# Kernel optimization log

Hardware: AMD Instinct MI355X
Metric: run time of the kernel (lower is better)

## Reference

```python
import jax, jax.numpy as jnp
import numpy as np

E = 8          # num_experts
TOP_K = 2
CAP_RATIO = 1.2


def setup_inputs() -> dict:
    key = jax.random.key(0)
    k1, k2, k3, k4 = jax.random.split(key, 4)
    B, L, D, H = 2, 2048, 768, 2048
    x = jax.random.normal(k1, (B, L, D), dtype=jnp.float32)
    Wg = jax.random.normal(k2, (D, E), dtype=jnp.float32) * 0.02   # gate: Linear(D, E, bias=False)
    W1 = jax.random.normal(k3, (E, D, 2 * H), dtype=jnp.float32) * 0.02  # fc1 per expert (y | gate halves)
    W2 = jax.random.normal(k4, (E, H, D), dtype=jnp.float32) * 0.02      # fc2 per expert
    return {"x": x, "Wg": Wg, "W1": W1, "W2": W2}


def reference(x, Wg, W1, W2):
    B, L, D = x.shape
    H = W2.shape[1]
    xf = x.reshape(-1, D)                      # [N, D]
    N = xf.shape[0]
    capacity = int(CAP_RATIO * N / E)          # static, matches torch int()

    logits = xf @ Wg                           # [N, E]
    scores, idx = jax.lax.top_k(logits, TOP_K) # [N, K] (descending, like torch.topk)
    weights = jax.nn.softmax(scores, axis=-1)  # [N, K]

    # padded token table: row N is a zero token used for unfilled capacity slots
    xpad = jnp.concatenate([xf, jnp.zeros((1, D), xf.dtype)], axis=0)
    wpad_zero = jnp.zeros((1,), weights.dtype)
    out = jnp.zeros((N, D), x.dtype)

    for k in range(TOP_K):
        ik = idx[:, k]                                         # [N] expert id per token
        onehot = (ik[:, None] == jnp.arange(E)[None, :])       # [N, E]
        pos = jnp.cumsum(onehot, axis=0) - 1                   # rank within expert, ascending token order
        posk = jnp.take_along_axis(pos, ik[:, None], axis=1)[:, 0]  # [N]
        keep = posk < capacity                                 # first-come capacity (== indices[:capacity])

        # dispatch buffer [E, C]: token index per slot, N (pad) where unfilled/dropped
        buf = jnp.full((E, capacity), N, dtype=jnp.int32)
        buf = buf.at[ik, posk].set(jnp.arange(N, dtype=jnp.int32), mode="drop")

        xg = xpad[buf]                                         # [E, C, D]
        h = jnp.einsum("ecd,edh->ech", xg, W1)                 # [E, C, 2H]
        act = h[..., :H] * jax.nn.silu(h[..., H:])             # GatedMLP: y * silu(gate)
        ye = jnp.einsum("ech,ehd->ecd", act, W2)               # [E, C, D]

        wk = jnp.where(keep, weights[:, k], 0.0)               # [N]
        w_buf = jnp.concatenate([wk, wpad_zero])[buf]          # [E, C], 0 on pad slots
        out = out.at[buf.reshape(-1)].add(
            (w_buf[..., None] * ye).reshape(E * capacity, D), mode="drop"
        )

    return out.reshape(B, L, D)
```

## Files before the change

kernel.cpp:

```cpp
#include <hip/hip_runtime.h>


typedef _Float16 half8 __attribute__((ext_vector_type(8)));
typedef _Float16 half4t __attribute__((ext_vector_type(4)));
typedef float f4 __attribute__((ext_vector_type(4)));

#define N_TOK 4096
#define DDIM  768
#define HDIM  2048
#define NEXP  8
#define CAP   614
#define CAPP  640

#define XH_OFF    0L
#define W1T_OFF   6292992L
#define W2T_OFF   56624640L
#define ACT_OFF   81790464L
#define EIDX_OFF  123733504L
#define WTS_OFF   123766272L
#define TOKL_OFF  123799040L
#define CNT_OFF   123840000L

__device__ __forceinline__ void gld16(const void* g, void* l) {
  __builtin_amdgcn_global_load_lds(
      (const __attribute__((address_space(1))) unsigned int*)g,
      (__attribute__((address_space(3))) unsigned int*)l, 16, 0, 0);
}

__device__ __forceinline__ void cvt2_tile(const float* __restrict__ src,
                                          _Float16* __restrict__ dst,
                                          int R, int C, int e, int r0, int c0,
                                          float* __restrict__ tile) {
  long sb = (long)e * R * C;
  int t = threadIdx.x;
  int rrow = t >> 4, c4 = (t & 15) * 4;
#pragma unroll
  for (int h = 0; h < 2; h++)
#pragma unroll
    for (int i = 0; i < 4; i++) {
      int row = i * 16 + rrow;
      f4 v = *(const f4*)(src + sb + (long)(r0 + row) * C + c0 + h * 64 + c4);
      *(f4*)(&tile[h * 4416 + row * 69 + c4]) = v;
    }
  __syncthreads();
#pragma unroll
  for (int h = 0; h < 2; h++)
#pragma unroll
    for (int s = 0; s < 2; s++) {
      int idx = t + s * 256;
      int c = idx >> 3, ch = idx & 7;
      half8 hv;
#pragma unroll
      for (int j = 0; j < 8; j++) hv[j] = (_Float16)tile[h * 4416 + (ch * 8 + j) * 69 + c];
      *(half8*)(dst + sb + (long)(c0 + h * 64 + c) * R + r0 + ch * 8) = hv;
    }
}

__global__ __launch_bounds__(256) void prep1_kernel(const float* __restrict__ W1,
                                                    const float* __restrict__ x,
                                                    const float* __restrict__ Wg,
                                                    _Float16* __restrict__ w1t,
                                                    _Float16* __restrict__ xh,
                                                    int* __restrict__ eidx,
                                                    float* __restrict__ wts) {
  __shared__ float smem[2 * 4416];
  int b = blockIdx.x;

  if (b < 3072) {
    int e = b / 384, rem = b % 384;
    int cx = rem % 12, cy = rem / 12;
    cvt2_tile(W1, w1t, 768, 4096, e, cx * 64, cy * 128, smem);
    return;
  }

  int rb = b - 3072;
  int t = threadIdx.x;
  for (int i = t; i < DDIM * NEXP; i += 256) smem[(i & 7) * DDIM + (i >> 3)] = Wg[i];
  __syncthreads();
  int w = t >> 6, lane = t & 63;
  int tok = rb * 4 + w;
  if (tok > N_TOK) return;
  if (tok == N_TOK) {
    half4t zz; zz[0] = zz[1] = zz[2] = zz[3] = (_Float16)0.f;
#pragma unroll
    for (int j = 0; j < 3; j++) *(half4t*)(xh + (long)N_TOK * DDIM + (lane + j * 64) * 4) = zz;
    return;
  }
  const float* xr = x + (long)tok * DDIM;
#pragma unroll
  for (int j = 0; j < 3; j++) {
    f4 v = *(const f4*)(xr + (lane + j * 64) * 4);
    half4t hv;
    hv[0] = (_Float16)v[0]; hv[1] = (_Float16)v[1];
    hv[2] = (_Float16)v[2]; hv[3] = (_Float16)v[3];
    *(half4t*)(xh + (long)tok * DDIM + (lane + j * 64) * 4) = hv;
  }
  float acc[8] = {0.f, 0.f, 0.f, 0.f, 0.f, 0.f, 0.f, 0.f};
#pragma unroll
  for (int i = 0; i < 12; i++) {
    float xv = xr[i * 64 + lane];
#pragma unroll
    for (int e2 = 0; e2 < 8; e2++) acc[e2] += xv * smem[e2 * DDIM + i * 64 + lane];
  }
#pragma unroll
  for (int e2 = 0; e2 < 8; e2++) {
    float v = acc[e2];
    v += __shfl_xor(v, 32); v += __shfl_xor(v, 16); v += __shfl_xor(v, 8);
    v += __shfl_xor(v, 4);  v += __shfl_xor(v, 2);  v += __shfl_xor(v, 1);
    acc[e2] = v;
  }
  if (lane == 0) {
    float m0 = -1e30f; int i0 = 0;
#pragma unroll
    for (int e2 = 0; e2 < 8; e2++) if (acc[e2] > m0) { m0 = acc[e2]; i0 = e2; }
    float m1 = -1e30f; int i1 = 0;
#pragma unroll
    for (int e2 = 0; e2 < 8; e2++) if (e2 != i0 && acc[e2] > m1) { m1 = acc[e2]; i1 = e2; }
    float tt = __expf(m1 - m0);
    float w0 = 1.f / (1.f + tt);
    eidx[tok * 2 + 0] = i0; eidx[tok * 2 + 1] = i1;
    wts[tok * 2 + 0] = w0;  wts[tok * 2 + 1] = 1.f - w0;
  }
}

__global__ __launch_bounds__(64) void scan_kernel(const int* __restrict__ eidx,
                                                  int* __restrict__ toklist,
                                                  int* __restrict__ counts) {
  int z = blockIdx.x;
  int k = z >> 3, e = z & 7;
  int lane = threadIdx.x;
  int mye[64];
#pragma unroll
  for (int c = 0; c < 64; c++) mye[c] = eidx[(c * 64 + lane) * 2 + k];
  int base = 0;
#pragma unroll 4
  for (int c = 0; c < 64; c++) {
    int n = c * 64 + lane;
    bool pred = (mye[c] == e);
    unsigned long long mask = __ballot(pred);
    if (pred) {
      int pos = base + __popcll(mask & ((1ull << lane) - 1ull));
      if (pos < CAP) toklist[z * CAPP + pos] = n;
    }
    base += __popcll(mask);
  }
  if (lane == 0) counts[z] = (base < CAP) ? base : CAP;
}

__global__ __launch_bounds__(256, 2) void gemm1_kernel(const _Float16* __restrict__ xh,
                                                       const _Float16* __restrict__ w1t,
                                                       const float* __restrict__ W2,
                                                       _Float16* __restrict__ w2t,
                                                       const int* __restrict__ toklist,
                                                       const int* __restrict__ counts,
                                                       _Float16* __restrict__ act) {
  __shared__ char smem[49664];

  int i = blockIdx.x;
  if (i >= 1280) {
    int b2 = i - 1280;
    int e = b2 / 192, rem = b2 % 192;
    int cx = rem % 32, cy = rem / 32;
    cvt2_tile(W2, w2t, 2048, 768, e, cx * 64, cy * 128, (float*)smem);
    return;
  }

  _Float16* As = (_Float16*)smem;
  _Float16* Bs = (_Float16*)(smem + 16384);
  int* toks = (int*)(smem + 49152);

  int xcd = i & 7, j = i >> 3;
  int m = j % 5, ii = j / 5;
  int k = ii & 1, n = ii >> 1;
  int e = xcd, z = k * 8 + e;
  int count = counts[z];
  int m0 = m * 128;
  if (m0 >= count) return;
  int n0 = n * 128;

  int t = threadIdx.x;
  if (t < 128) {
    int r = m0 + t;
    toks[t] = (r < count) ? toklist[z * CAPP + r] : N_TOK;
  }
  __syncthreads();

  int lane = t & 63, w = t >> 6;
  int l8 = lane >> 3, u8 = lane & 7;

  const _Float16* ag[4]; _Float16* al[4];
#pragma unroll
  for (int s = 0; s < 4; s++) {
    int row = w * 32 + s * 8 + l8;
    ag[s] = xh + (long)toks[row] * DDIM + ((u8 ^ (row & 7)) * 8);
    al[s] = As + row * 64 + u8 * 8;
  }
  const _Float16* bg[8]; _Float16* bl[8];
#pragma unroll
  for (int s = 0; s < 8; s++) {
    int rb = w * 64 + s * 8 + l8;
    int gr = (rb < 128) ? (n0 + rb) : (2048 + n0 + (rb - 128));
    bg[s] = w1t + ((long)e * 4096 + gr) * DDIM + ((u8 ^ (rb & 7)) * 8);
    bl[s] = Bs + rb * 64 + u8 * 8;
  }

  int q = lane >> 4, m16 = lane & 15;
  int wm = w & 1, wn = w >> 1;

  f4 zero4 = {0.f, 0.f, 0.f, 0.f};
  f4 acc[4][4][2];
#pragma unroll
  for (int rt = 0; rt < 4; rt++)
#pragma unroll
    for (int ct = 0; ct < 4; ct++) { acc[rt][ct][0] = zero4; acc[rt][ct][1] = zero4; }

  for (int kk = 0; kk < DDIM; kk += 64) {
    __syncthreads();
#pragma unroll
    for (int s = 0; s < 4; s++) { gld16(ag[s], al[s]); ag[s] += 64; }
#pragma unroll
    for (int s = 0; s < 8; s++) { gld16(bg[s], bl[s]); bg[s] += 64; }
    __syncthreads();

#pragma unroll
    for (int c = 0; c < 2; c++) {
      half8 af[4], bf[4][2];
#pragma unroll
      for (int rt = 0; rt < 4; rt++) {
        int row = wm * 64 + rt * 16 + m16;
        af[rt] = *(const half8*)(As + row * 64 + (((c * 4 + q) ^ (row & 7)) * 8));
      }
#pragma unroll
      for (int ct = 0; ct < 4; ct++) {
        int cb = wn * 64 + ct * 16 + m16;
        int ph = ((c * 4 + q) ^ (cb & 7)) * 8;
        bf[ct][0] = *(const half8*)(Bs + cb * 64 + ph);
        bf[ct][1] = *(const half8*)(Bs + (128 + cb) * 64 + ph);
      }
#pragma unroll
      for (int rt = 0; rt < 4; rt++)
#pragma unroll
        for (int ct = 0; ct < 4; ct++) {
          acc[rt][ct][0] = __builtin_amdgcn_mfma_f32_16x16x32_f16(af[rt], bf[ct][0], acc[rt][ct][0], 0, 0, 0);
          acc[rt][ct][1] = __builtin_amdgcn_mfma_f32_16x16x32_f16(af[rt], bf[ct][1], acc[rt][ct][1], 0, 0, 0);
        }
    }
  }

  long ab = (long)z * CAPP * HDIM;
#pragma unroll
  for (int rt = 0; rt < 4; rt++)
#pragma unroll
    for (int ct = 0; ct < 4; ct++)
#pragma unroll
      for (int r = 0; r < 4; r++) {
        int row = m0 + wm * 64 + rt * 16 + q * 4 + r;
        int col = n0 + wn * 64 + ct * 16 + m16;
        float h1 = acc[rt][ct][0][r], h2 = acc[rt][ct][1][r];
        float s = h2 / (1.f + __expf(-h2));
        act[ab + (long)row * HDIM + col] = (_Float16)(h1 * s);
      }
}

__global__ __launch_bounds__(256, 3) void gemm2_kernel(const _Float16* __restrict__ act,
                                                       const _Float16* __restrict__ w2t,
                                                       const int* __restrict__ toklist,
                                                       const int* __restrict__ counts,
                                                       const float* __restrict__ wts,
                                                       float* __restrict__ out) {
  int i = blockIdx.x;
  int xcd = i & 7, j = i >> 3;
  int m = j % 5, t2 = j / 5;
  int k = t2 & 1, n = t2 >> 1;
  int e = xcd, z = k * 8 + e;
  int count = counts[z];
  int m0 = m * 128;
  if (m0 >= count) return;
  int n0 = n * 128;

  __shared__ _Float16 As[128 * 64];
  __shared__ _Float16 Bs[128 * 64];
  __shared__ int toksL[128];
  __shared__ float wrow[128];

  int t = threadIdx.x;
  if (t < 128) {
    int r = m0 + t;
    if (r < count) {
      int tok = toklist[z * CAPP + r];
      toksL[t] = tok;
      wrow[t] = wts[tok * 2 + k];
    } else {
      toksL[t] = -1;
      wrow[t] = 0.f;
    }
  }
  __syncthreads();

  int lane = t & 63, w = t >> 6;
  int l8 = lane >> 3, u8 = lane & 7;

  const _Float16* ag[4]; _Float16* al[4];
#pragma unroll
  for (int s = 0; s < 4; s++) {
    int row = w * 32 + s * 8 + l8;
    ag[s] = act + ((long)z * CAPP + m0 + row) * HDIM + ((u8 ^ (row & 7)) * 8);
    al[s] = As + row * 64 + u8 * 8;
  }
  const _Float16* bg[4]; _Float16* bl[4];
#pragma unroll
  for (int s = 0; s < 4; s++) {
    int rb = w * 32 + s * 8 + l8;
    bg[s] = w2t + ((long)e * DDIM + n0 + rb) * HDIM + ((u8 ^ (rb & 7)) * 8);
    bl[s] = Bs + rb * 64 + u8 * 8;
  }

  int q = lane >> 4, m16 = lane & 15;
  int wm = w & 1, wn = w >> 1;

  f4 zero4 = {0.f, 0.f, 0.f, 0.f};
  f4 acc[4][4];
#pragma unroll
  for (int rt = 0; rt < 4; rt++)
#pragma unroll
    for (int ct = 0; ct < 4; ct++) acc[rt][ct] = zero4;

  for (int kk = 0; kk < HDIM; kk += 64) {
    __syncthreads();
#pragma unroll
    for (int s = 0; s < 4; s++) { gld16(ag[s], al[s]); ag[s] += 64; }
#pragma unroll
    for (int s = 0; s < 4; s++) { gld16(bg[s], bl[s]); bg[s] += 64; }
    __syncthreads();

#pragma unroll
    for (int c = 0; c < 2; c++) {
      half8 af[4], bf[4];
#pragma unroll
      for (int rt = 0; rt < 4; rt++) {
        int row = wm * 64 + rt * 16 + m16;
        af[rt] = *(const half8*)(As + row * 64 + (((c * 4 + q) ^ (row & 7)) * 8));
      }
#pragma unroll
      for (int ct = 0; ct < 4; ct++) {
        int cb = wn * 64 + ct * 16 + m16;
        bf[ct] = *(const half8*)(Bs + cb * 64 + (((c * 4 + q) ^ (cb & 7)) * 8));
      }
#pragma unroll
      for (int rt = 0; rt < 4; rt++)
#pragma unroll
        for (int ct = 0; ct < 4; ct++)
          acc[rt][ct] = __builtin_amdgcn_mfma_f32_16x16x32_f16(af[rt], bf[ct], acc[rt][ct], 0, 0, 0);
    }
  }

#pragma unroll
  for (int rt = 0; rt < 4; rt++)
#pragma unroll
    for (int ct = 0; ct < 4; ct++)
#pragma unroll
      for (int r = 0; r < 4; r++) {
        int lr = wm * 64 + rt * 16 + q * 4 + r;
        int tok = toksL[lr];
        if (tok >= 0) {
          int col = n0 + wn * 64 + ct * 16 + m16;
          atomicAdd(&out[(long)tok * DDIM + col], wrow[lr] * acc[rt][ct][r]);
        }
      }
}


extern "C" void kernel_launch(void* const* d_in, const int* in_sizes, int n_in,
                              void* d_out, int out_size, void* d_ws, size_t ws_size,
                              hipStream_t stream) {
  const float* x  = (const float*)d_in[0];
  const float* Wg = (const float*)d_in[1];
  const float* W1 = (const float*)d_in[2];
  const float* W2 = (const float*)d_in[3];
  float* out = (float*)d_out;
  char* ws = (char*)d_ws;

  _Float16* xh   = (_Float16*)(ws + XH_OFF);
  _Float16* w1t  = (_Float16*)(ws + W1T_OFF);
  _Float16* w2t  = (_Float16*)(ws + W2T_OFF);
  _Float16* actb = (_Float16*)(ws + ACT_OFF);
  int* eidx      = (int*)(ws + EIDX_OFF);
  float* wts     = (float*)(ws + WTS_OFF);
  int* toklist   = (int*)(ws + TOKL_OFF);
  int* counts    = (int*)(ws + CNT_OFF);

  hipMemsetAsync(d_out, 0, (size_t)out_size * sizeof(float), stream);
  prep1_kernel<<<4097, 256, 0, stream>>>(W1, x, Wg, w1t, xh, eidx, wts);
  scan_kernel<<<16, 64, 0, stream>>>(eidx, toklist, counts);
  gemm1_kernel<<<2816, 256, 0, stream>>>(xh, w1t, W2, w2t, toklist, counts, actb);
  gemm2_kernel<<<480, 256, 0, stream>>>(actb, w2t, toklist, counts, wts, out);
}
```

Before: 332.0 us.

## Replace atomic scatter with slot buffer plus gather; use per-wave weight transposes

gemm2 now writes unweighted expert outputs to a dense slot buffer, and a new gather kernel uses an inverse token-to-slot map from the scan to combine both top-k contributions per token. This removes the output memset and the float atomics. The weight fp32-to-fp16 transpose now runs one tile per wave without block-wide syncs. gemm1 also interleaves W2 conversion blocks with GEMM blocks to overlap them. The cost is an extra kernel launch and a round trip of the fp32 slot buffer through memory. The slot buffer reuses the W1T region, which appears to be safe because w1t is dead by the time gemm2 runs.

```diff
diff --git a/kernel.cpp b/kernel.cpp
--- a/kernel.cpp
+++ b/kernel.cpp
@@ -14,12 +14,14 @@
 
 #define XH_OFF    0L
 #define W1T_OFF   6292992L
+#define YB_OFF    6292992L
 #define W2T_OFF   56624640L
 #define ACT_OFF   81790464L
 #define EIDX_OFF  123733504L
 #define WTS_OFF   123766272L
 #define TOKL_OFF  123799040L
 #define CNT_OFF   123840000L
+#define INV_OFF   123840256L
 
 __device__ __forceinline__ void gld16(const void* g, void* l) {
   __builtin_amdgcn_global_load_lds(
@@ -27,33 +29,50 @@
       (__attribute__((address_space(3))) unsigned int*)l, 16, 0, 0);
 }
 
-__device__ __forceinline__ void cvt2_tile(const float* __restrict__ src,
-                                          _Float16* __restrict__ dst,
-                                          int R, int C, int e, int r0, int c0,
-                                          float* __restrict__ tile) {
+__device__ __forceinline__ void cvt_wave64(const float* __restrict__ src,
+                                           _Float16* __restrict__ dst,
+                                           int R, int C, int e, int r0, int c0,
+                                           float* __restrict__ wt, int lane) {
   long sb = (long)e * R * C;
-  int t = threadIdx.x;
-  int rrow = t >> 4, c4 = (t & 15) * 4;
-#pragma unroll
-  for (int h = 0; h < 2; h++)
-#pragma unroll
-    for (int i = 0; i < 4; i++) {
-      int row = i * 16 + rrow;
-      f4 v = *(const f4*)(src + sb + (long)(r0 + row) * C + c0 + h * 64 + c4);
-      *(f4*)(&tile[h * 4416 + row * 69 + c4]) = v;
-    }
-  __syncthreads();
-#pragma unroll
-  for (int h = 0; h < 2; h++)
-#pragma unroll
-    for (int s = 0; s < 2; s++) {
-      int idx = t + s * 256;
-      int c = idx >> 3, ch = idx & 7;
-      half8 hv;
-#pragma unroll
-      for (int j = 0; j < 8; j++) hv[j] = (_Float16)tile[h * 4416 + (ch * 8 + j) * 69 + c];
-      *(half8*)(dst + sb + (long)(c0 + h * 64 + c) * R + r0 + ch * 8) = hv;
-    }
+  int lr = lane >> 4, l4 = (lane & 15) * 4;
+#pragma unroll
+  for (int s = 0; s < 16; s++) {
+    int row = s * 4 + lr;
+    f4 v = *(const f4*)(src + sb + (long)(r0 + row) * C + c0 + l4);
+    *(f4*)(&wt[row * 68 + l4]) = v;
+  }
+  asm volatile("s_waitcnt lgkmcnt(0)" ::: "memory");
+  int c = lane;
+#pragma unroll
+  for (int ch = 0; ch < 8; ch++) {
+    half8 h;
+#pragma unroll
+    for (int j = 0; j < 8; j++) h[j] = (_Float16)wt[(ch * 8 + j) * 68 + c];
+    *(half8*)(dst + sb + (long)(c0 + c) * R + r0 + ch * 8) = h;
+  }
+}
+
+__device__ __forceinline__ void cvt_wave32(const float* __restrict__ src,
+                                           _Float16* __restrict__ dst,
+                                           int R, int C, int e, int r0, int c0,
+                                           float* __restrict__ wt, int lane) {
+  long sb = (long)e * R * C;
+  int r8 = lane >> 3, l4 = (lane & 7) * 4;
+#pragma unroll
+  for (int s = 0; s < 8; s++) {
+    int row = s * 8 + r8;
+    f4 v = *(const f4*)(src + sb + (long)(r0 + row) * C + c0 + l4);
+    *(f4*)(&wt[row * 36 + l4]) = v;
+  }
+  asm volatile("s_waitcnt lgkmcnt(0)" ::: "memory");
+  int c = lane & 31, h2 = lane >> 5;
+#pragma unroll
+  for (int ch = 0; ch < 4; ch++) {
+    half8 h;
+#pragma unroll
+    for (int j = 0; j < 8; j++) h[j] = (_Float16)wt[(h2 * 32 + ch * 8 + j) * 36 + c];
+    *(half8*)(dst + sb + (long)(c0 + c) * R + r0 + h2 * 32 + ch * 8) = h;
+  }
 }
 
 __global__ __launch_bounds__(256) void prep1_kernel(const float* __restrict__ W1,
@@ -63,22 +82,22 @@
                                                     _Float16* __restrict__ xh,
                                                     int* __restrict__ eidx,
                                                     float* __restrict__ wts) {
-  __shared__ float smem[2 * 4416];
+  __shared__ float pls[4 * 64 * 68];
   int b = blockIdx.x;
-
-  if (b < 3072) {
-    int e = b / 384, rem = b % 384;
+  int t = threadIdx.x;
+  int w = t >> 6, lane = t & 63;
+
+  if (b >= 1025) {
+    int cb = b - 1025;
+    int e = cb / 192, rem = cb % 192;
     int cx = rem % 12, cy = rem / 12;
-    cvt2_tile(W1, w1t, 768, 4096, e, cx * 64, cy * 128, smem);
+    cvt_wave64(W1, w1t, 768, 4096, e, cx * 64, cy * 256 + w * 64, pls + w * (64 * 68), lane);
     return;
   }
 
-  int rb = b - 3072;
-  int t = threadIdx.x;
-  for (int i = t; i < DDIM * NEXP; i += 256) smem[(i & 7) * DDIM + (i >> 3)] = Wg[i];
+  for (int i = t; i < DDIM * NEXP; i += 256) pls[(i & 7) * DDIM + (i >> 3)] = Wg[i];
   __syncthreads();
-  int w = t >> 6, lane = t & 63;
-  int tok = rb * 4 + w;
+  int tok = b * 4 + w;
   if (tok > N_TOK) return;
   if (tok == N_TOK) {
     half4t zz; zz[0] = zz[1] = zz[2] = zz[3] = (_Float16)0.f;
@@ -100,7 +119,7 @@
   for (int i = 0; i < 12; i++) {
     float xv = xr[i * 64 + lane];
 #pragma unroll
-    for (int e2 = 0; e2 < 8; e2++) acc[e2] += xv * smem[e2 * DDIM + i * 64 + lane];
+    for (int e2 = 0; e2 < 8; e2++) acc[e2] += xv * pls[e2 * DDIM + i * 64 + lane];
   }
 #pragma unroll
   for (int e2 = 0; e2 < 8; e2++) {
@@ -125,7 +144,8 @@
 
 __global__ __launch_bounds__(64) void scan_kernel(const int* __restrict__ eidx,
                                                   int* __restrict__ toklist,
-                                                  int* __restrict__ counts) {
+                                                  int* __restrict__ counts,
+                                                  int* __restrict__ inv) {
   int z = blockIdx.x;
   int k = z >> 3, e = z & 7;
   int lane = threadIdx.x;
@@ -140,7 +160,12 @@
     unsigned long long mask = __ballot(pred);
     if (pred) {
       int pos = base + __popcll(mask & ((1ull << lane) - 1ull));
-      if (pos < CAP) toklist[z * CAPP + pos] = n;
+      if (pos < CAP) {
+        toklist[z * CAPP + pos] = n;
+        inv[n * 2 + k] = z * CAPP + pos;
+      } else {
+        inv[n * 2 + k] = -1;
+      }
     }
     base += __popcll(mask);
   }
@@ -154,22 +179,27 @@
                                                        const int* __restrict__ toklist,
                                                        const int* __restrict__ counts,
                                                        _Float16* __restrict__ act) {
-  __shared__ char smem[49664];
-
+  __shared__ float smemf[12416];
+
+  int t = threadIdx.x;
   int i = blockIdx.x;
-  if (i >= 1280) {
-    int b2 = i - 1280;
-    int e = b2 / 192, rem = b2 % 192;
-    int cx = rem % 32, cy = rem / 32;
-    cvt2_tile(W2, w2t, 2048, 768, e, cx * 64, cy * 128, (float*)smem);
+  int gi = -1, ci = -1;
+  if (i < 2560) { int g = i >> 4, r = i & 15; if (r < 8) gi = g * 8 + r; else ci = g * 8 + (r - 8); }
+  else ci = 1280 + (i - 2560);
+
+  if (ci >= 0) {
+    int e = ci / 192, rem = ci % 192;
+    int cx = rem % 32, cc = rem / 32;
+    int w = t >> 6, lane = t & 63;
+    cvt_wave32(W2, w2t, 2048, 768, e, cx * 64, cc * 128 + w * 32, smemf + w * 2304, lane);
     return;
   }
 
-  _Float16* As = (_Float16*)smem;
-  _Float16* Bs = (_Float16*)(smem + 16384);
-  int* toks = (int*)(smem + 49152);
-
-  int xcd = i & 7, j = i >> 3;
+  _Float16* As = (_Float16*)smemf;
+  _Float16* Bs = (_Float16*)(smemf + 4096);
+  int* toks = (int*)(smemf + 12288);
+
+  int xcd = gi & 7, j = gi >> 3;
   int m = j % 5, ii = j / 5;
   int k = ii & 1, n = ii >> 1;
   int e = xcd, z = k * 8 + e;
@@ -178,7 +208,6 @@
   if (m0 >= count) return;
   int n0 = n * 128;
 
-  int t = threadIdx.x;
   if (t < 128) {
     int r = m0 + t;
     toks[t] = (r < count) ? toklist[z * CAPP + r] : N_TOK;
@@ -264,10 +293,8 @@
 
 __global__ __launch_bounds__(256, 3) void gemm2_kernel(const _Float16* __restrict__ act,
                                                        const _Float16* __restrict__ w2t,
-                                                       const int* __restrict__ toklist,
                                                        const int* __restrict__ counts,
-                                                       const float* __restrict__ wts,
-                                                       float* __restrict__ out) {
+                                                       float* __restrict__ ybuf) {
   int i = blockIdx.x;
   int xcd = i & 7, j = i >> 3;
   int m = j % 5, t2 = j / 5;
@@ -280,23 +307,8 @@
 
   __shared__ _Float16 As[128 * 64];
   __shared__ _Float16 Bs[128 * 64];
-  __shared__ int toksL[128];
-  __shared__ float wrow[128];
 
   int t = threadIdx.x;
-  if (t < 128) {
-    int r = m0 + t;
-    if (r < count) {
-      int tok = toklist[z * CAPP + r];
-      toksL[t] = tok;
-      wrow[t] = wts[tok * 2 + k];
-    } else {
-      toksL[t] = -1;
-      wrow[t] = 0.f;
-    }
-  }
-  __syncthreads();
-
   int lane = t & 63, w = t >> 6;
   int l8 = lane >> 3, u8 = lane & 7;
 
@@ -361,12 +373,50 @@
 #pragma unroll
       for (int r = 0; r < 4; r++) {
         int lr = wm * 64 + rt * 16 + q * 4 + r;
-        int tok = toksL[lr];
-        if (tok >= 0) {
-          int col = n0 + wn * 64 + ct * 16 + m16;
-          atomicAdd(&out[(long)tok * DDIM + col], wrow[lr] * acc[rt][ct][r]);
-        }
-      }
+        int col = n0 + wn * 64 + ct * 16 + m16;
+        ybuf[((long)z * CAPP + m0 + lr) * DDIM + col] = acc[rt][ct][r];
+      }
+}
+
+__global__ __launch_bounds__(256) void gather_kernel(const float* __restrict__ ybuf,
+                                                     const int* __restrict__ inv,
+                                                     const float* __restrict__ wts,
+                                                     float* __restrict__ out) {
+  int t = threadIdx.x;
+  int w = t >> 6, lane = t & 63;
+  int tok = blockIdx.x * 4 + w;
+  int s0 = inv[tok * 2 + 0], s1 = inv[tok * 2 + 1];
+  float w0 = wts[tok * 2 + 0], w1 = wts[tok * 2 + 1];
+  float acc[12];
+#pragma unroll
+  for (int j = 0; j < 12; j++) acc[j] = 0.f;
+  int b = lane * 12;
+  if (s0 >= 0) {
+    const float* y = ybuf + (long)s0 * DDIM + b;
+#pragma unroll
+    for (int v = 0; v < 3; v++) {
+      f4 qv = *(const f4*)(y + v * 4);
+#pragma unroll
+      for (int j = 0; j < 4; j++) acc[v * 4 + j] += w0 * qv[j];
+    }
+  }
+  if (s1 >= 0) {
+    const float* y = ybuf + (long)s1 * DDIM + b;
+#pragma unroll
+    for (int v = 0; v < 3; v++) {
+      f4 qv = *(const f4*)(y + v * 4);
+#pragma unroll
+      for (int j = 0; j < 4; j++) acc[v * 4 + j] += w1 * qv[j];
+    }
+  }
+  float* o = out + (long)tok * DDIM + b;
+#pragma unroll
+  for (int v = 0; v < 3; v++) {
+    f4 qv;
+#pragma unroll
+    for (int j = 0; j < 4; j++) qv[j] = acc[v * 4 + j];
+    *(f4*)(o + v * 4) = qv;
+  }
 }
 
 
@@ -382,16 +432,18 @@
 
   _Float16* xh   = (_Float16*)(ws + XH_OFF);
   _Float16* w1t  = (_Float16*)(ws + W1T_OFF);
+  float*    ybuf = (float*)(ws + YB_OFF);
   _Float16* w2t  = (_Float16*)(ws + W2T_OFF);
   _Float16* actb = (_Float16*)(ws + ACT_OFF);
   int* eidx      = (int*)(ws + EIDX_OFF);
   float* wts     = (float*)(ws + WTS_OFF);
   int* toklist   = (int*)(ws + TOKL_OFF);
   int* counts    = (int*)(ws + CNT_OFF);
-
-  hipMemsetAsync(d_out, 0, (size_t)out_size * sizeof(float), stream);
-  prep1_kernel<<<4097, 256, 0, stream>>>(W1, x, Wg, w1t, xh, eidx, wts);
-  scan_kernel<<<16, 64, 0, stream>>>(eidx, toklist, counts);
+  int* inv       = (int*)(ws + INV_OFF);
+
+  prep1_kernel<<<2561, 256, 0, stream>>>(W1, x, Wg, w1t, xh, eidx, wts);
+  scan_kernel<<<16, 64, 0, stream>>>(eidx, toklist, counts, inv);
   gemm1_kernel<<<2816, 256, 0, stream>>>(xh, w1t, W2, w2t, toklist, counts, actb);
-  gemm2_kernel<<<480, 256, 0, stream>>>(actb, w2t, toklist, counts, wts, out);
-}
+  gemm2_kernel<<<480, 256, 0, stream>>>(actb, w2t, counts, ybuf);
+  gather_kernel<<<1024, 256, 0, stream>>>(ybuf, inv, wts, out);
+}
```

Measured after the change: 377.1 us. 13.6% more time.

## Replace gemm2 atomic scatter with slot buffer and per-token gather combine

Applied to the files above, without the earlier changes.

gemm2 now writes its fp32 expert outputs to a dense per-slot buffer, reusing the W1 fp16 workspace region, instead of doing weighted atomicAdds into the output. The scan kernel also records an inverse map from each (token, k) pair to its slot. A new gather kernel then reads both slots per token, applies the routing weights and writes the output directly, so the output memset goes away. This trades scattered atomics for an extra round-trip of a roughly 31 MB buffer and one more kernel launch.

```diff
diff --git a/kernel.cpp b/kernel.cpp
--- a/kernel.cpp
+++ b/kernel.cpp
@@ -14,12 +14,14 @@
 
 #define XH_OFF    0L
 #define W1T_OFF   6292992L
+#define YB_OFF    6292992L
 #define W2T_OFF   56624640L
 #define ACT_OFF   81790464L
 #define EIDX_OFF  123733504L
 #define WTS_OFF   123766272L
 #define TOKL_OFF  123799040L
 #define CNT_OFF   123840000L
+#define INV_OFF   123840256L
 
 __device__ __forceinline__ void gld16(const void* g, void* l) {
   __builtin_amdgcn_global_load_lds(
@@ -125,7 +127,8 @@
 
 __global__ __launch_bounds__(64) void scan_kernel(const int* __restrict__ eidx,
                                                   int* __restrict__ toklist,
-                                                  int* __restrict__ counts) {
+                                                  int* __restrict__ counts,
+                                                  int* __restrict__ inv) {
   int z = blockIdx.x;
   int k = z >> 3, e = z & 7;
   int lane = threadIdx.x;
@@ -140,7 +143,12 @@
     unsigned long long mask = __ballot(pred);
     if (pred) {
       int pos = base + __popcll(mask & ((1ull << lane) - 1ull));
-      if (pos < CAP) toklist[z * CAPP + pos] = n;
+      if (pos < CAP) {
+        toklist[z * CAPP + pos] = n;
+        inv[n * 2 + k] = z * CAPP + pos;
+      } else {
+        inv[n * 2 + k] = -1;
+      }
     }
     base += __popcll(mask);
   }
@@ -264,10 +272,8 @@
 
 __global__ __launch_bounds__(256, 3) void gemm2_kernel(const _Float16* __restrict__ act,
                                                        const _Float16* __restrict__ w2t,
-                                                       const int* __restrict__ toklist,
                                                        const int* __restrict__ counts,
-                                                       const float* __restrict__ wts,
-                                                       float* __restrict__ out) {
+                                                       float* __restrict__ ybuf) {
   int i = blockIdx.x;
   int xcd = i & 7, j = i >> 3;
   int m = j % 5, t2 = j / 5;
@@ -280,23 +286,8 @@
 
   __shared__ _Float16 As[128 * 64];
   __shared__ _Float16 Bs[128 * 64];
-  __shared__ int toksL[128];
-  __shared__ float wrow[128];
 
   int t = threadIdx.x;
-  if (t < 128) {
-    int r = m0 + t;
-    if (r < count) {
-      int tok = toklist[z * CAPP + r];
-      toksL[t] = tok;
-      wrow[t] = wts[tok * 2 + k];
-    } else {
-      toksL[t] = -1;
-      wrow[t] = 0.f;
-    }
-  }
-  __syncthreads();
-
   int lane = t & 63, w = t >> 6;
   int l8 = lane >> 3, u8 = lane & 7;
 
@@ -361,12 +352,50 @@
 #pragma unroll
       for (int r = 0; r < 4; r++) {
         int lr = wm * 64 + rt * 16 + q * 4 + r;
-        int tok = toksL[lr];
-        if (tok >= 0) {
-          int col = n0 + wn * 64 + ct * 16 + m16;
-          atomicAdd(&out[(long)tok * DDIM + col], wrow[lr] * acc[rt][ct][r]);
-        }
-      }
+        int col = n0 + wn * 64 + ct * 16 + m16;
+        ybuf[((long)z * CAPP + m0 + lr) * DDIM + col] = acc[rt][ct][r];
+      }
+}
+
+__global__ __launch_bounds__(256) void gather_kernel(const float* __restrict__ ybuf,
+                                                     const int* __restrict__ inv,
+                                                     const float* __restrict__ wts,
+                                                     float* __restrict__ out) {
+  int t = threadIdx.x;
+  int w = t >> 6, lane = t & 63;
+  int tok = blockIdx.x * 4 + w;
+  int s0 = inv[tok * 2 + 0], s1 = inv[tok * 2 + 1];
+  float w0 = wts[tok * 2 + 0], w1 = wts[tok * 2 + 1];
+  float acc[12];
+#pragma unroll
+  for (int j = 0; j < 12; j++) acc[j] = 0.f;
+  int b = lane * 12;
+  if (s0 >= 0) {
+    const float* y = ybuf + (long)s0 * DDIM + b;
+#pragma unroll
+    for (int v = 0; v < 3; v++) {
+      f4 qv = *(const f4*)(y + v * 4);
+#pragma unroll
+      for (int j = 0; j < 4; j++) acc[v * 4 + j] += w0 * qv[j];
+    }
+  }
+  if (s1 >= 0) {
+    const float* y = ybuf + (long)s1 * DDIM + b;
+#pragma unroll
+    for (int v = 0; v < 3; v++) {
+      f4 qv = *(const f4*)(y + v * 4);
+#pragma unroll
+      for (int j = 0; j < 4; j++) acc[v * 4 + j] += w1 * qv[j];
+    }
+  }
+  float* o = out + (long)tok * DDIM + b;
+#pragma unroll
+  for (int v = 0; v < 3; v++) {
+    f4 qv;
+#pragma unroll
+    for (int j = 0; j < 4; j++) qv[j] = acc[v * 4 + j];
+    *(f4*)(o + v * 4) = qv;
+  }
 }
 
 
@@ -382,16 +411,18 @@
 
   _Float16* xh   = (_Float16*)(ws + XH_OFF);
   _Float16* w1t  = (_Float16*)(ws + W1T_OFF);
+  float*    ybuf = (float*)(ws + YB_OFF);
   _Float16* w2t  = (_Float16*)(ws + W2T_OFF);
   _Float16* actb = (_Float16*)(ws + ACT_OFF);
   int* eidx      = (int*)(ws + EIDX_OFF);
   float* wts     = (float*)(ws + WTS_OFF);
   int* toklist   = (int*)(ws + TOKL_OFF);
   int* counts    = (int*)(ws + CNT_OFF);
-
-  hipMemsetAsync(d_out, 0, (size_t)out_size * sizeof(float), stream);
+  int* inv       = (int*)(ws + INV_OFF);
+
   prep1_kernel<<<4097, 256, 0, stream>>>(W1, x, Wg, w1t, xh, eidx, wts);
-  scan_kernel<<<16, 64, 0, stream>>>(eidx, toklist, counts);
+  scan_kernel<<<16, 64, 0, stream>>>(eidx, toklist, counts, inv);
   gemm1_kernel<<<2816, 256, 0, stream>>>(xh, w1t, W2, w2t, toklist, counts, actb);
-  gemm2_kernel<<<480, 256, 0, stream>>>(actb, w2t, toklist, counts, wts, out);
-}
+  gemm2_kernel<<<480, 256, 0, stream>>>(actb, w2t, counts, ybuf);
+  gather_kernel<<<1024, 256, 0, stream>>>(ybuf, inv, wts, out);
+}
```

New measurement: 331.3 us. Within noise of the previous version (-0.2%).
